# Optimization experiments

Hardware: AMD Instinct MI355X
Metric: run time of the kernel (lower is better)

Reference implementation:

```python
import jax, jax.numpy as jnp
import numpy as np

B, N, E = 2, 2048, 2048
H, D = 16, 128
BASE = 10000.0


def rope(t, offset=0):
    # t: [b, n, h, d] -- rotary position embedding (Lrpe type 1), half-rotation form
    d = t.shape[-1]
    pos = jnp.arange(t.shape[1], dtype=jnp.float32) + offset
    inv = BASE ** (-jnp.arange(0, d, 2, dtype=jnp.float32) / d)  # [d/2]
    ang = pos[:, None] * inv[None, :]                            # [n, d/2]
    cos = jnp.cos(ang)[None, :, None, :]
    sin = jnp.sin(ang)[None, :, None, :]
    t1, t2 = t[..., : d // 2], t[..., d // 2 :]
    return jnp.concatenate([t1 * cos - t2 * sin, t2 * cos + t1 * sin], axis=-1)


def setup_inputs() -> dict:
    key = jax.random.key(0)
    ks = jax.random.split(key, 6)
    s = lambda k, shape, fan: jax.random.normal(k, shape, jnp.float32) / np.sqrt(fan)
    return {
        "x": jax.random.normal(ks[0], (B, N, E), jnp.float32),
        "Wq": s(ks[1], (H * D, E), E),      # q_proj.weight
        "Wkv": s(ks[2], (2 * D, E), E),     # kv_proj.weight
        "Wkvh": s(ks[3], (2 * H, E), E),    # kv_head_proj.weight
        "Wg": s(ks[4], (2 * H, E), E),      # gate_proj.weight (gate_type=1)
        "Wout": s(ks[5], (E, H * D), H * D) # out_proj.weight
    }


def reference(x, Wq, Wkv, Wkvh, Wg, Wout):
    b, n, _ = x.shape
    q = (x @ Wq.T).reshape(b, n, H, D)
    kv = x @ Wkv.T            # [b, n, 2D]
    kv_head = x @ Wkvh.T      # [b, n, 2H] (mpa_type=0, activation 'none')

    # gate_type == 1: log-sigmoid gated cumulative-sum decay on kv_head (GLA-style)
    g = x @ Wg.T                                                       # [b, n, 2H]
    log_f = jnp.concatenate(
        [jnp.zeros((b, 1, 2 * H), jnp.float32), jax.nn.log_sigmoid(g)], axis=1
    )
    log_f_cumsum = jnp.cumsum(log_f, axis=1)[:, :-1]                   # [b, n, 2H]
    kv_head = kv_head * jnp.exp(log_f_cumsum)
    kv_head = jnp.cumsum(kv_head, axis=1)

    kp, vp = kv[..., :D], kv[..., D:]
    kh, vh = kv_head[..., :H], kv_head[..., H:]
    # low-rank KV expansion: outer product of shared (d) with per-head scalar (h)
    k = jnp.einsum('bnd,bnh->bnhd', kp, kh)
    v = jnp.einsum('bnd,bnh->bnhd', vp, vh)

    q = rope(q)
    k = rope(k)

    # causal softmax attention (flash_attn_func equivalent), scale = D**-0.5
    scale = 1.0 / np.sqrt(D)
    scores = jnp.einsum('bnhd,bmhd->bhnm', q, k) * scale
    mask = jnp.tril(jnp.ones((n, n), bool))
    scores = jnp.where(mask[None, None], scores, -jnp.inf)
    p = jax.nn.softmax(scores, axis=-1)
    o = jnp.einsum('bhnm,bmhd->bnhd', p, v).reshape(b, n, H * D)
    return o @ Wout.T
```

## Files before the change

### kernel.cpp

```cpp
#include <hip/hip_runtime.h>
#include <hip/hip_bf16.h>
#include <math.h>

typedef __attribute__((ext_vector_type(8))) short bf16x8;
typedef __attribute__((ext_vector_type(4))) float f32x4;

#define MFMA16(a, b, c) __builtin_amdgcn_mfma_f32_16x16x32_bf16((a), (b), (c), 0, 0, 0)

static __device__ __forceinline__ float fast_exp2(float x) { return __builtin_amdgcn_exp2f(x); }

static __device__ __forceinline__ unsigned short f2bf(float f) {
  __hip_bfloat16 h = __float2bfloat16(f);
  unsigned short u;
  __builtin_memcpy(&u, &h, 2);
  return u;
}
static __device__ __forceinline__ float bf2f(unsigned short u) {
  unsigned int x = ((unsigned int)u) << 16;
  float f;
  __builtin_memcpy(&f, &x, 4);
  return f;
}

static __device__ __forceinline__ void cast8(const float* __restrict__ src,
                                             unsigned short* __restrict__ dst, int blk, int tid) {
  int i = (blk * 256 + tid) * 8;
  float4 a = *(const float4*)(src + i);
  float4 b = *(const float4*)(src + i + 4);
  union { unsigned short u[8]; bf16x8 v; } o;
  o.u[0] = f2bf(a.x); o.u[1] = f2bf(a.y); o.u[2] = f2bf(a.z); o.u[3] = f2bf(a.w);
  o.u[4] = f2bf(b.x); o.u[5] = f2bf(b.y); o.u[6] = f2bf(b.z); o.u[7] = f2bf(b.w);
  *(bf16x8*)(dst + i) = o.v;
}

__global__ __launch_bounds__(256) void prep(const float* __restrict__ x, const float* __restrict__ Wq,
                                            const float* __restrict__ Wout, const float* __restrict__ Wkv,
                                            const float* __restrict__ Wkvh, const float* __restrict__ Wg,
                                            unsigned short* __restrict__ x_bf, unsigned short* __restrict__ wq_bf,
                                            unsigned short* __restrict__ wout_bf, unsigned short* __restrict__ wsm_bf,
                                            float2* __restrict__ cs, float* __restrict__ wgt) {
  int bid = blockIdx.x, tid = threadIdx.x;
  if (bid < 4096) {
    cast8(x, x_bf, bid, tid);
  } else if (bid < 6144) {
    cast8(Wq, wq_bf, bid - 4096, tid);
  } else if (bid < 8192) {
    cast8(Wout, wout_bf, bid - 6144, tid);
  } else if (bid < 8576) {
    int row = bid - 8192;
    int c = tid * 8;
    const float* src = nullptr;
    if (row < 256) src = Wkv + (size_t)row * 2048;
    else if (row < 288) src = Wkvh + (size_t)(row - 256) * 2048;
    union { unsigned short u[8]; bf16x8 v; } o;
    if (src) {
      float4 a = *(const float4*)(src + c);
      float4 b = *(const float4*)(src + c + 4);
      o.u[0] = f2bf(a.x); o.u[1] = f2bf(a.y); o.u[2] = f2bf(a.z); o.u[3] = f2bf(a.w);
      o.u[4] = f2bf(b.x); o.u[5] = f2bf(b.y); o.u[6] = f2bf(b.z); o.u[7] = f2bf(b.w);
    } else {
      for (int j = 0; j < 8; j++) o.u[j] = 0;
    }
    *(bf16x8*)(wsm_bf + (size_t)row * 2048 + c) = o.v;
  } else if (bid < 9088) {
    int i = (bid - 8576) * 256 + tid;
    int f = i & 63, n = i >> 6;
    float inv = powf(10000.0f, -(float)(2 * f) / 128.0f);
    float ang = (float)n * inv;
    cs[i] = make_float2(cosf(ang), sinf(ang));
  } else {
    int i = (bid - 9088) * 256 + tid;
    int oc = i >> 11, k = i & 2047;
    wgt[(size_t)k * 32 + oc] = Wg[i];
  }
}

__global__ __launch_bounds__(256) void gproj(const float* __restrict__ x, const float* __restrict__ Wgt,
                                             float* __restrict__ lsg_t) {
  int tid = blockIdx.x * 256 + threadIdx.x;
  int tok = tid >> 5, oc = tid & 31;
  const float* xr = x + (size_t)tok * 2048;
  float acc = 0.f;
  for (int k = 0; k < 2048; k += 4) {
    float4 a = *(const float4*)(xr + k);
    acc += a.x * Wgt[(size_t)k * 32 + oc] + a.y * Wgt[(size_t)(k + 1) * 32 + oc] +
           a.z * Wgt[(size_t)(k + 2) * 32 + oc] + a.w * Wgt[(size_t)(k + 3) * 32 + oc];
  }
  float ls = (acc >= 0.f) ? -log1pf(expf(-acc)) : acc - log1pf(expf(acc));
  int b = tok >> 11, n = tok & 2047;
  lsg_t[((size_t)(b * 32 + oc)) * 2048 + n] = ls;
}

__global__ __launch_bounds__(256) void scan_kernel(const float* __restrict__ lsg_t,
                                                   const float* __restrict__ so,
                                                   float* __restrict__ khvh) {
  int b = blockIdx.x >> 5, ch = blockIdx.x & 31;
  int t = threadIdx.x, lane = t & 63, wv = t >> 6;
  const float* L = lsg_t + ((size_t)(b * 32 + ch)) * 2048 + t * 8;
  float ls[8], v[8];
  float4 a = *(const float4*)L, c = *(const float4*)(L + 4);
  ls[0] = a.x; ls[1] = a.y; ls[2] = a.z; ls[3] = a.w;
  ls[4] = c.x; ls[5] = c.y; ls[6] = c.z; ls[7] = c.w;
  const float* V = so + ((size_t)(b * 2048 + t * 8)) * 384 + 256 + ch;
#pragma unroll
  for (int j = 0; j < 8; j++) v[j] = V[(size_t)j * 384];
  float run = 0.f;
#pragma unroll
  for (int j = 0; j < 8; j++) run += ls[j];
  float incl = run;
#pragma unroll
  for (int off = 1; off < 64; off <<= 1) {
    float nv = __shfl_up(incl, off);
    if (lane >= off) incl += nv;
  }
  __shared__ float ws[2][4];
  if (lane == 63) ws[0][wv] = incl;
  __syncthreads();
  float wbase = 0.f;
#pragma unroll
  for (int w = 0; w < 4; w++) wbase += (w < wv) ? ws[0][w] : 0.f;
  float baseA = wbase + incl - run;
  float lf = baseA, s = 0.f;
#pragma unroll
  for (int j = 0; j < 8; j++) { s += v[j] * __expf(lf); lf += ls[j]; }
  float incl2 = s;
#pragma unroll
  for (int off = 1; off < 64; off <<= 1) {
    float nv = __shfl_up(incl2, off);
    if (lane >= off) incl2 += nv;
  }
  if (lane == 63) ws[1][wv] = incl2;
  __syncthreads();
  float wbase2 = 0.f;
#pragma unroll
  for (int w = 0; w < 4; w++) wbase2 += (w < wv) ? ws[1][w] : 0.f;
  float base2 = wbase2 + incl2 - s;
  lf = baseA; s = base2;
  float* O = khvh + ((size_t)(b * 2048 + t * 8)) * 32 + ch;
#pragma unroll
  for (int j = 0; j < 8; j++) { s += v[j] * __expf(lf); lf += ls[j]; O[(size_t)j * 32] = s; }
}

__global__ __launch_bounds__(256) void build_kv2(const float* __restrict__ so,
                                                 const float* __restrict__ khvh,
                                                 const float2* __restrict__ cs,
                                                 unsigned short* __restrict__ k_r,
                                                 unsigned short* __restrict__ v_t) {
  int ntb = blockIdx.x, bh = blockIdx.y;
  int b = bh >> 4, h = bh & 15;
  int tok0 = b * 2048 + ntb * 64;
  int n0 = ntb * 64;
  __shared__ float khs[64], vhs[64];
  __shared__ unsigned short Vt_s[64 * 132];
  int t = threadIdx.x;
  if (t < 64) {
    khs[t] = khvh[(size_t)(tok0 + t) * 32 + h];
    vhs[t] = khvh[(size_t)(tok0 + t) * 32 + 16 + h];
  }
  __syncthreads();
#pragma unroll
  for (int c = 0; c < 4; c++) {
    int idx = c * 256 + t;
    int r = idx >> 4, q4 = (idx & 15) * 4;
    const float* sop = so + (size_t)(tok0 + r) * 384;
    float4 k1 = *(const float4*)(sop + q4);
    float4 k2 = *(const float4*)(sop + 64 + q4);
    float kh = khs[r];
    int n = n0 + r;
    union { unsigned short u[4]; uint2 v2; } o1, o2;
#pragma unroll
    for (int j = 0; j < 4; j++) {
      float2 cc = cs[(n << 6) + q4 + j];
      float av = ((const float*)&k1)[j], bv = ((const float*)&k2)[j];
      o1.u[j] = f2bf((av * cc.x - bv * cc.y) * kh);
      o2.u[j] = f2bf((bv * cc.x + av * cc.y) * kh);
    }
    size_t off = ((size_t)bh * 2048 + n) * 128 + q4;
    *(uint2*)(k_r + off) = o1.v2;
    *(uint2*)(k_r + off + 64) = o2.v2;
  }
#pragma unroll
  for (int c = 0; c < 8; c++) {
    int idx = c * 256 + t;
    int r = idx >> 5, d4 = (idx & 31) * 4;
    const float* sop = so + (size_t)(tok0 + r) * 384 + 128;
    float4 v = *(const float4*)(sop + d4);
    float vh = vhs[r];
    union { unsigned short u[4]; uint2 v2; } ov;
#pragma unroll
    for (int j = 0; j < 4; j++) ov.u[j] = f2bf(((const float*)&v)[j] * vh);
    *(uint2*)&Vt_s[r * 132 + d4] = ov.v2;
  }
  __syncthreads();
#pragma unroll
  for (int c = 0; c < 4; c++) {
    int idx = c * 256 + t;
    int d = idx >> 3, c8 = (idx & 7) * 8;
    union { unsigned short u[8]; bf16x8 v; } o;
#pragma unroll
    for (int j = 0; j < 8; j++) o.u[j] = Vt_s[(c8 + j) * 132 + d];
    *(bf16x8*)(v_t + ((size_t)bh * 128 + d) * 2048 + n0 + c8) = o.v;
  }
}

template <int MODE>
__global__ __launch_bounds__(256) void gemm_bt(const unsigned short* __restrict__ A,
                                               const unsigned short* __restrict__ B,
                                               float* __restrict__ Cf,
                                               unsigned short* __restrict__ Cb,
                                               int K, int ldc) {
  __shared__ unsigned short As[128 * 32];
  __shared__ unsigned short Bs[128 * 32];
  int tid = threadIdx.x;
  int wave = tid >> 6, lane = tid & 63, l15 = lane & 15, lg = lane >> 4;
  int wr = wave >> 1, wc = wave & 1;
  int lin = blockIdx.y * gridDim.x + blockIdx.x;
  int cpx = (gridDim.x * gridDim.y) >> 3;
  int swz = (lin & 7) * cpx + (lin >> 3);
  int bx = swz % gridDim.x, by = swz / gridDim.x;
  int row0 = by * 128, col0 = bx * 128;
  f32x4 acc[4][4];
#pragma unroll
  for (int m = 0; m < 4; m++)
#pragma unroll
    for (int n = 0; n < 4; n++) acc[m][n] = (f32x4){0.f, 0.f, 0.f, 0.f};

  for (int k0 = 0; k0 < K; k0 += 32) {
#pragma unroll
    for (int c = 0; c < 2; c++) {
      int chunk = c * 256 + tid;
      int r = chunk >> 2, kk = (chunk & 3) * 8;
      __builtin_amdgcn_global_load_lds(
          (const __attribute__((address_space(1))) void*)(A + (size_t)(row0 + r) * K + k0 + kk),
          (__attribute__((address_space(3))) void*)(As + ((size_t)c * 256 + wave * 64) * 8), 16, 0, 0);
      __builtin_amdgcn_global_load_lds(
          (const __attribute__((address_space(1))) void*)(B + (size_t)(col0 + r) * K + k0 + kk),
          (__attribute__((address_space(3))) void*)(Bs + ((size_t)c * 256 + wave * 64) * 8), 16, 0, 0);
    }
    __syncthreads();
    bf16x8 af[4], bfr[4];
#pragma unroll
    for (int m = 0; m < 4; m++) af[m] = *(const bf16x8*)&As[(wr * 64 + m * 16 + l15) * 32 + lg * 8];
#pragma unroll
    for (int n = 0; n < 4; n++) bfr[n] = *(const bf16x8*)&Bs[(wc * 64 + n * 16 + l15) * 32 + lg * 8];
#pragma unroll
    for (int m = 0; m < 4; m++)
#pragma unroll
      for (int n = 0; n < 4; n++) acc[m][n] = MFMA16(af[m], bfr[n], acc[m][n]);
    __syncthreads();
  }

  if (MODE == 0 || col0 >= 2048) {
#pragma unroll
    for (int m = 0; m < 4; m++) {
      int row_b = row0 + wr * 64 + m * 16 + lg * 4;
#pragma unroll
      for (int n = 0; n < 4; n++) {
        int col = col0 + wc * 64 + n * 16 + l15;
        int cw = (MODE == 0) ? col : (col - 2048);
#pragma unroll
        for (int j = 0; j < 4; j++) {
          Cf[(size_t)(row_b + j) * ldc + cw] = acc[m][n][j];
        }
      }
    }
  } else {
#pragma unroll
    for (int m = 0; m < 4; m++) {
      int row_b = row0 + wr * 64 + m * 16 + lg * 4;
#pragma unroll
      for (int n = 0; n < 4; n++) {
        int col = col0 + wc * 64 + n * 16 + l15;
        int h = col >> 7, d = col & 127;
#pragma unroll
        for (int j = 0; j < 4; j++) {
          int row = row_b + j;
          int b = row >> 11, nn = row & 2047;
          Cb[(((size_t)b * 16 + h) * 2048 + nn) * 128 + d] = f2bf(acc[m][n][j]);
        }
      }
    }
  }
}

__global__ __launch_bounds__(256, 2) void flash_attn(const unsigned short* __restrict__ q_r,
                                                     const unsigned short* __restrict__ k_r,
                                                     const unsigned short* __restrict__ v_t,
                                                     const float2* __restrict__ cs,
                                                     unsigned short* __restrict__ o) {
  int lin = blockIdx.y * 16 + blockIdx.x;
  int swz = (lin & 7) * 64 + (lin >> 3);
  int bx = swz & 15, bh = swz >> 4;
  const unsigned short* Kg = k_r + (size_t)bh * 2048 * 128;
  const unsigned short* Vtg = v_t + (size_t)bh * 128 * 2048;
  __shared__ unsigned short Ks[2][64 * 128];
  __shared__ unsigned short VTs[2][128 * 64];
  __shared__ unsigned short Ps[4][16 * 80];
  int tid = threadIdx.x, wave = tid >> 6, lane = tid & 63, l15 = lane & 15, lg = lane >> 4;
  int sw = (l15 & 7) * 8;
  int b = bh >> 4, h = bh & 15;

  union { unsigned short u[8]; bf16x8 v; } onesu;
#pragma unroll
  for (int j = 0; j < 8; j++) onesu.u[j] = 0x3F80;
  const bf16x8 ones = onesu.v;

  int qtA = bx, qtB = 31 - bx;
  int qt = qtA;

  bf16x8 qf[4];
#define LOAD_Q()                                                                                   \
  {                                                                                                \
    const unsigned short* Qg = q_r + ((size_t)bh * 2048 + qt * 64) * 128;                          \
    int n = qt * 64 + wave * 16 + l15;                                                             \
    union { unsigned short u[8]; bf16x8 v; } r0, r1, r2, r3;                                       \
    r0.v = *(const bf16x8*)(Qg + (wave * 16 + l15) * 128 + 0 * 32 + lg * 8);                       \
    r1.v = *(const bf16x8*)(Qg + (wave * 16 + l15) * 128 + 1 * 32 + lg * 8);                       \
    r2.v = *(const bf16x8*)(Qg + (wave * 16 + l15) * 128 + 2 * 32 + lg * 8);                       \
    r3.v = *(const bf16x8*)(Qg + (wave * 16 + l15) * 128 + 3 * 32 + lg * 8);                       \
    union { unsigned short u[8]; bf16x8 v; } o0, o1, o2, o3;                                       \
    _Pragma("unroll") for (int j = 0; j < 8; j++) {                                                \
      float2 c0 = cs[(n << 6) + 0 * 32 + lg * 8 + j];                                              \
      float t1 = bf2f(r0.u[j]), t2 = bf2f(r2.u[j]);                                                \
      o0.u[j] = f2bf(t1 * c0.x - t2 * c0.y);                                                       \
      o2.u[j] = f2bf(t2 * c0.x + t1 * c0.y);                                                       \
      float2 c1 = cs[(n << 6) + 1 * 32 + lg * 8 + j];                                              \
      float s1 = bf2f(r1.u[j]), s2 = bf2f(r3.u[j]);                                                \
      o1.u[j] = f2bf(s1 * c1.x - s2 * c1.y);                                                       \
      o3.u[j] = f2bf(s2 * c1.x + s1 * c1.y);                                                       \
    }                                                                                              \
    qf[0] = o0.v; qf[1] = o1.v; qf[2] = o2.v; qf[3] = o3.v;                                        \
  }

  LOAD_Q();

  float m_r[4], l_r[4];
  f32x4 oacc[8];
#pragma unroll
  for (int j = 0; j < 4; j++) { m_r[j] = -INFINITY; l_r[j] = 0.f; }
#pragma unroll
  for (int db = 0; db < 8; db++) oacc[db] = (f32x4){0.f, 0.f, 0.f, 0.f};

  const float kscale = 0.12753102f;
  const float THR = 11.0f;

#define STAGE(kt, bsel)                                                                           \
  {                                                                                               \
    int kti = (kt);                                                                               \
    int bs = (bsel);                                                                              \
    _Pragma("unroll") for (int c = 0; c < 4; c++) {                                               \
      int s = c * 256 + tid;                                                                      \
      int kr = s >> 4, kc = ((s & 15) ^ (kr & 7)) * 8;                                            \
      __builtin_amdgcn_global_load_lds(                                                           \
          (const __attribute__((address_space(1))) void*)(Kg + (size_t)(kti * 64 + kr) * 128 + kc),\
          (__attribute__((address_space(3))) void*)(&Ks[bs][(c * 256 + wave * 64) * 8]), 16, 0, 0);\
      int vr = s >> 3, vc = ((s & 7) ^ (vr & 7)) * 8;                                             \
      __builtin_amdgcn_global_load_lds(                                                           \
          (const __attribute__((address_space(1))) void*)(Vtg + (size_t)vr * 2048 + kti * 64 + vc),\
          (__attribute__((address_space(3))) void*)(&VTs[bs][(c * 256 + wave * 64) * 8]), 16, 0, 0);\
    }                                                                                             \
  }

  STAGE(0, 0);
  __syncthreads();

  for (int s = 0; s < 33; ++s) {
    int nb = s & 1;
    if (s + 1 < 33) {
      int nk = (s + 1 <= qtA) ? (s + 1) : (s + 1 - (qtA + 1));
      STAGE(nk, nb ^ 1);
    }
    int kt = (s <= qtA) ? s : (s - (qtA + 1));
    bool diag = (s == qtA) || (s == 32);
    int qrow0 = qt * 64 + wave * 16 + lg * 4;

    f32x4 sc[4];
#pragma unroll
    for (int cb = 0; cb < 4; cb++) sc[cb] = (f32x4){0.f, 0.f, 0.f, 0.f};
    __builtin_amdgcn_s_setprio(1);
#pragma unroll
    for (int kk = 0; kk < 4; kk++) {
#pragma unroll
      for (int cb = 0; cb < 4; cb++) {
        bf16x8 kf = *(const bf16x8*)&Ks[nb][(cb * 16 + l15) * 128 + ((kk * 32 + lg * 8) ^ sw)];
        sc[cb] = MFMA16(qf[kk], kf, sc[cb]);
      }
    }
    __builtin_amdgcn_s_setprio(0);
    if (diag) {
#pragma unroll
      for (int cb = 0; cb < 4; cb++) {
        int col = kt * 64 + cb * 16 + l15;
#pragma unroll
        for (int j = 0; j < 4; j++) {
          float v = sc[cb][j] * kscale;
          if (col > qrow0 + j) v = -INFINITY;
          sc[cb][j] = v;
        }
      }
    } else {
#pragma unroll
      for (int cb = 0; cb < 4; cb++)
#pragma unroll
        for (int j = 0; j < 4; j++) sc[cb][j] *= kscale;
    }
    float pm[4];
#pragma unroll
    for (int j = 0; j < 4; j++)
      pm[j] = fmaxf(fmaxf(sc[0][j], sc[1][j]), fmaxf(sc[2][j], sc[3][j]));
    bool grow = !__all((pm[0] <= m_r[0] + THR) & (pm[1] <= m_r[1] + THR) &
                       (pm[2] <= m_r[2] + THR) & (pm[3] <= m_r[3] + THR));
    if (grow) {
#pragma unroll
      for (int off = 1; off < 16; off <<= 1) {
#pragma unroll
        for (int j = 0; j < 4; j++) pm[j] = fmaxf(pm[j], __shfl_xor(pm[j], off));
      }
#pragma unroll
      for (int j = 0; j < 4; j++) {
        float mn = fmaxf(m_r[j], pm[j]);
        float corr = fast_exp2(m_r[j] - mn);
        m_r[j] = mn;
        l_r[j] *= corr;
#pragma unroll
        for (int db = 0; db < 8; db++) oacc[db][j] *= corr;
      }
    }
#pragma unroll
    for (int cb = 0; cb < 4; cb++)
#pragma unroll
      for (int j = 0; j < 4; j++)
        Ps[wave][(lg * 4 + j) * 80 + cb * 16 + l15] = f2bf(fast_exp2(sc[cb][j] - m_r[j]));
    f32x4 sacc = (f32x4){0.f, 0.f, 0.f, 0.f};
    __builtin_amdgcn_s_setprio(1);
#pragma unroll
    for (int kc = 0; kc < 2; kc++) {
      bf16x8 pa = *(const bf16x8*)&Ps[wave][l15 * 80 + kc * 32 + lg * 8];
      sacc = MFMA16(pa, ones, sacc);
#pragma unroll
      for (int db = 0; db < 8; db++) {
        bf16x8 vb = *(const bf16x8*)&VTs[nb][(db * 16 + l15) * 64 + ((kc * 32 + lg * 8) ^ sw)];
        oacc[db] = MFMA16(pa, vb, oacc[db]);
      }
    }
    __builtin_amdgcn_s_setprio(0);
#pragma unroll
    for (int j = 0; j < 4; j++) l_r[j] += sacc[j];
    __syncthreads();

    if (s == qtA) {
      int qrow_e = qt * 64 + wave * 16 + lg * 4;
#pragma unroll
      for (int db = 0; db < 8; db++) {
        int d = db * 16 + l15;
#pragma unroll
        for (int j = 0; j < 4; j++) {
          float val = oacc[db][j] / l_r[j];
          o[((size_t)(b * 2048 + qrow_e + j)) * 2048 + h * 128 + d] = f2bf(val);
        }
      }
      qt = qtB;
      LOAD_Q();
#pragma unroll
      for (int j = 0; j < 4; j++) { m_r[j] = -INFINITY; l_r[j] = 0.f; }
#pragma unroll
      for (int db = 0; db < 8; db++) oacc[db] = (f32x4){0.f, 0.f, 0.f, 0.f};
    }
  }
  int qrow_e = qt * 64 + wave * 16 + lg * 4;
#pragma unroll
  for (int db = 0; db < 8; db++) {
    int d = db * 16 + l15;
#pragma unroll
    for (int j = 0; j < 4; j++) {
      float val = oacc[db][j] / l_r[j];
      o[((size_t)(b * 2048 + qrow_e + j)) * 2048 + h * 128 + d] = f2bf(val);
    }
  }
#undef STAGE
#undef LOAD_Q
}

extern "C" void kernel_launch(void* const* d_in, const int* in_sizes, int n_in,
                              void* d_out, int out_size, void* d_ws, size_t ws_size,
                              hipStream_t stream) {
  (void)in_sizes; (void)n_in; (void)out_size; (void)ws_size;
  const float* x    = (const float*)d_in[0];
  const float* Wq   = (const float*)d_in[1];
  const float* Wkv  = (const float*)d_in[2];
  const float* Wkvh = (const float*)d_in[3];
  const float* Wg   = (const float*)d_in[4];
  const float* Wout = (const float*)d_in[5];
  float* out = (float*)d_out;

  char* ws = (char*)d_ws;
  size_t off = 0;
  auto alloc = [&](size_t bytes) -> void* {
    void* p = ws + off;
    off += (bytes + 255) & ~(size_t)255;
    return p;
  };
  unsigned short* x_bf    = (unsigned short*)alloc(4096ull * 2048 * 2);
  unsigned short* wq_bf   = (unsigned short*)alloc(2048ull * 2048 * 2);
  unsigned short* wsm_bf  = (unsigned short*)alloc(384ull * 2048 * 2);
  unsigned short* wout_bf = (unsigned short*)alloc(2048ull * 2048 * 2);
  unsigned short* q_r     = (unsigned short*)alloc(4096ull * 2048 * 2);
  unsigned short* k_r     = (unsigned short*)alloc(4096ull * 2048 * 2);
  unsigned short* o_bf    = (unsigned short*)alloc(4096ull * 2048 * 2);
  float* small_out        = (float*)alloc(4096ull * 384 * 4);
  float* lsg_t            = (float*)alloc(64ull * 2048 * 4);
  float* khvh             = (float*)alloc(4096ull * 32 * 4);
  float2* cs              = (float2*)alloc(2048ull * 64 * 8);
  float* wgt              = (float*)alloc(2048ull * 32 * 4);
  unsigned short* v_t     = x_bf;

  prep<<<9344, 256, 0, stream>>>(x, Wq, Wout, Wkv, Wkvh, Wg, x_bf, wq_bf, wout_bf, wsm_bf, cs, wgt);
  gproj<<<512, 256, 0, stream>>>(x, wgt, lsg_t);
  gemm_bt<1><<<dim3(19, 32), 256, 0, stream>>>(x_bf, wq_bf, small_out, q_r, 2048, 384);
  scan_kernel<<<64, 256, 0, stream>>>(lsg_t, small_out, khvh);
  build_kv2<<<dim3(32, 32), 256, 0, stream>>>(small_out, khvh, cs, k_r, v_t);
  flash_attn<<<dim3(16, 32), 256, 0, stream>>>(q_r, k_r, v_t, cs, o_bf);
  gemm_bt<0><<<dim3(16, 32), 256, 0, stream>>>(o_bf, wout_bf, out, nullptr, 2048, 2048);
}
```

Before: 284.0 us.

## Merge gate projection into Q GEMM launch and deepen GEMM K tile

```diff
diff --git a/kernel.cpp b/kernel.cpp
--- a/kernel.cpp
+++ b/kernel.cpp
@@ -75,20 +75,121 @@
   }
 }
 
-__global__ __launch_bounds__(256) void gproj(const float* __restrict__ x, const float* __restrict__ Wgt,
-                                             float* __restrict__ lsg_t) {
-  int tid = blockIdx.x * 256 + threadIdx.x;
-  int tok = tid >> 5, oc = tid & 31;
-  const float* xr = x + (size_t)tok * 2048;
-  float acc = 0.f;
-  for (int k = 0; k < 2048; k += 4) {
-    float4 a = *(const float4*)(xr + k);
-    acc += a.x * Wgt[(size_t)k * 32 + oc] + a.y * Wgt[(size_t)(k + 1) * 32 + oc] +
-           a.z * Wgt[(size_t)(k + 2) * 32 + oc] + a.w * Wgt[(size_t)(k + 3) * 32 + oc];
-  }
-  float ls = (acc >= 0.f) ? -log1pf(expf(-acc)) : acc - log1pf(expf(acc));
-  int b = tok >> 11, n = tok & 2047;
-  lsg_t[((size_t)(b * 32 + oc)) * 2048 + n] = ls;
+template <int MODE>
+static __device__ __forceinline__ void gemm_body(const unsigned short* __restrict__ A,
+                                                 const unsigned short* __restrict__ B,
+                                                 float* __restrict__ Cf,
+                                                 unsigned short* __restrict__ Cb,
+                                                 int K, int ldc, int lin, int nbx, int cpx) {
+  __shared__ unsigned short As[128 * 64];
+  __shared__ unsigned short Bs[128 * 64];
+  int tid = threadIdx.x;
+  int wave = tid >> 6, lane = tid & 63, l15 = lane & 15, lg = lane >> 4;
+  int wr = wave >> 1, wc = wave & 1;
+  int swz = (lin & 7) * cpx + (lin >> 3);
+  int bx = swz % nbx, by = swz / nbx;
+  int row0 = by * 128, col0 = bx * 128;
+  f32x4 acc[4][4];
+#pragma unroll
+  for (int m = 0; m < 4; m++)
+#pragma unroll
+    for (int n = 0; n < 4; n++) acc[m][n] = (f32x4){0.f, 0.f, 0.f, 0.f};
+
+  for (int k0 = 0; k0 < K; k0 += 64) {
+#pragma unroll
+    for (int c = 0; c < 4; c++) {
+      int chunk = c * 256 + tid;
+      int r = chunk >> 3, kk = (chunk & 7) * 8;
+      __builtin_amdgcn_global_load_lds(
+          (const __attribute__((address_space(1))) void*)(A + (size_t)(row0 + r) * K + k0 + kk),
+          (__attribute__((address_space(3))) void*)(As + ((size_t)c * 256 + wave * 64) * 8), 16, 0, 0);
+      __builtin_amdgcn_global_load_lds(
+          (const __attribute__((address_space(1))) void*)(B + (size_t)(col0 + r) * K + k0 + kk),
+          (__attribute__((address_space(3))) void*)(Bs + ((size_t)c * 256 + wave * 64) * 8), 16, 0, 0);
+    }
+    __syncthreads();
+    bf16x8 af[4][2], bfr[4][2];
+#pragma unroll
+    for (int m = 0; m < 4; m++)
+#pragma unroll
+      for (int ks = 0; ks < 2; ks++)
+        af[m][ks] = *(const bf16x8*)&As[(wr * 64 + m * 16 + l15) * 64 + ks * 32 + lg * 8];
+#pragma unroll
+    for (int n = 0; n < 4; n++)
+#pragma unroll
+      for (int ks = 0; ks < 2; ks++)
+        bfr[n][ks] = *(const bf16x8*)&Bs[(wc * 64 + n * 16 + l15) * 64 + ks * 32 + lg * 8];
+#pragma unroll
+    for (int ks = 0; ks < 2; ks++)
+#pragma unroll
+      for (int m = 0; m < 4; m++)
+#pragma unroll
+        for (int n = 0; n < 4; n++) acc[m][n] = MFMA16(af[m][ks], bfr[n][ks], acc[m][n]);
+    __syncthreads();
+  }
+
+  if (MODE == 0 || col0 >= 2048) {
+#pragma unroll
+    for (int m = 0; m < 4; m++) {
+      int row_b = row0 + wr * 64 + m * 16 + lg * 4;
+#pragma unroll
+      for (int n = 0; n < 4; n++) {
+        int col = col0 + wc * 64 + n * 16 + l15;
+        int cw = (MODE == 0) ? col : (col - 2048);
+#pragma unroll
+        for (int j = 0; j < 4; j++) {
+          Cf[(size_t)(row_b + j) * ldc + cw] = acc[m][n][j];
+        }
+      }
+    }
+  } else {
+#pragma unroll
+    for (int m = 0; m < 4; m++) {
+      int row_b = row0 + wr * 64 + m * 16 + lg * 4;
+#pragma unroll
+      for (int n = 0; n < 4; n++) {
+        int col = col0 + wc * 64 + n * 16 + l15;
+        int h = col >> 7, d = col & 127;
+#pragma unroll
+        for (int j = 0; j < 4; j++) {
+          int row = row_b + j;
+          int b = row >> 11, nn = row & 2047;
+          Cb[(((size_t)b * 16 + h) * 2048 + nn) * 128 + d] = f2bf(acc[m][n][j]);
+        }
+      }
+    }
+  }
+}
+
+__global__ __launch_bounds__(256) void gemm_q_gproj(const unsigned short* __restrict__ A,
+                                                    const unsigned short* __restrict__ B,
+                                                    float* __restrict__ small_out,
+                                                    unsigned short* __restrict__ q_r,
+                                                    const float* __restrict__ x,
+                                                    const float* __restrict__ Wgt,
+                                                    float* __restrict__ lsg_t) {
+  if (blockIdx.x >= 608) {
+    int tid = (blockIdx.x - 608) * 256 + threadIdx.x;
+    int tok = tid >> 5, oc = tid & 31;
+    const float* xr = x + (size_t)tok * 2048;
+    float acc = 0.f;
+    for (int k = 0; k < 2048; k += 4) {
+      float4 a = *(const float4*)(xr + k);
+      acc += a.x * Wgt[(size_t)k * 32 + oc] + a.y * Wgt[(size_t)(k + 1) * 32 + oc] +
+             a.z * Wgt[(size_t)(k + 2) * 32 + oc] + a.w * Wgt[(size_t)(k + 3) * 32 + oc];
+    }
+    float ls = (acc >= 0.f) ? -log1pf(expf(-acc)) : acc - log1pf(expf(acc));
+    int b = tok >> 11, n = tok & 2047;
+    lsg_t[((size_t)(b * 32 + oc)) * 2048 + n] = ls;
+    return;
+  }
+  gemm_body<1>(A, B, small_out, q_r, 2048, 384, blockIdx.x, 19, 76);
+}
+
+__global__ __launch_bounds__(256) void gemm_out(const unsigned short* __restrict__ A,
+                                                const unsigned short* __restrict__ B,
+                                                float* __restrict__ C) {
+  gemm_body<0>(A, B, C, nullptr, 2048, 2048, (int)(blockIdx.y * 16 + blockIdx.x), 16, 64);
 }
 
 __global__ __launch_bounds__(256) void scan_kernel(const float* __restrict__ lsg_t,
@@ -203,86 +304,6 @@
   }
 }
 
-template <int MODE>
-__global__ __launch_bounds__(256) void gemm_bt(const unsigned short* __restrict__ A,
-                                               const unsigned short* __restrict__ B,
-                                               float* __restrict__ Cf,
-                                               unsigned short* __restrict__ Cb,
-                                               int K, int ldc) {
-  __shared__ unsigned short As[128 * 32];
-  __shared__ unsigned short Bs[128 * 32];
-  int tid = threadIdx.x;
-  int wave = tid >> 6, lane = tid & 63, l15 = lane & 15, lg = lane >> 4;
-  int wr = wave >> 1, wc = wave & 1;
-  int lin = blockIdx.y * gridDim.x + blockIdx.x;
-  int cpx = (gridDim.x * gridDim.y) >> 3;
-  int swz = (lin & 7) * cpx + (lin >> 3);
-  int bx = swz % gridDim.x, by = swz / gridDim.x;
-  int row0 = by * 128, col0 = bx * 128;
-  f32x4 acc[4][4];
-#pragma unroll
-  for (int m = 0; m < 4; m++)
-#pragma unroll
-    for (int n = 0; n < 4; n++) acc[m][n] = (f32x4){0.f, 0.f, 0.f, 0.f};
-
-  for (int k0 = 0; k0 < K; k0 += 32) {
-#pragma unroll
-    for (int c = 0; c < 2; c++) {
-      int chunk = c * 256 + tid;
-      int r = chunk >> 2, kk = (chunk & 3) * 8;
-      __builtin_amdgcn_global_load_lds(
-          (const __attribute__((address_space(1))) void*)(A + (size_t)(row0 + r) * K + k0 + kk),
-          (__attribute__((address_space(3))) void*)(As + ((size_t)c * 256 + wave * 64) * 8), 16, 0, 0);
-      __builtin_amdgcn_global_load_lds(
-          (const __attribute__((address_space(1))) void*)(B + (size_t)(col0 + r) * K + k0 + kk),
-          (__attribute__((address_space(3))) void*)(Bs + ((size_t)c * 256 + wave * 64) * 8), 16, 0, 0);
-    }
-    __syncthreads();
-    bf16x8 af[4], bfr[4];
-#pragma unroll
-    for (int m = 0; m < 4; m++) af[m] = *(const bf16x8*)&As[(wr * 64 + m * 16 + l15) * 32 + lg * 8];
-#pragma unroll
-    for (int n = 0; n < 4; n++) bfr[n] = *(const bf16x8*)&Bs[(wc * 64 + n * 16 + l15) * 32 + lg * 8];
-#pragma unroll
-    for (int m = 0; m < 4; m++)
-#pragma unroll
-      for (int n = 0; n < 4; n++) acc[m][n] = MFMA16(af[m], bfr[n], acc[m][n]);
-    __syncthreads();
-  }
-
-  if (MODE == 0 || col0 >= 2048) {
-#pragma unroll
-    for (int m = 0; m < 4; m++) {
-      int row_b = row0 + wr * 64 + m * 16 + lg * 4;
-#pragma unroll
-      for (int n = 0; n < 4; n++) {
-        int col = col0 + wc * 64 + n * 16 + l15;
-        int cw = (MODE == 0) ? col : (col - 2048);
-#pragma unroll
-        for (int j = 0; j < 4; j++) {
-          Cf[(size_t)(row_b + j) * ldc + cw] = acc[m][n][j];
-        }
-      }
-    }
-  } else {
-#pragma unroll
-    for (int m = 0; m < 4; m++) {
-      int row_b = row0 + wr * 64 + m * 16 + lg * 4;
-#pragma unroll
-      for (int n = 0; n < 4; n++) {
-        int col = col0 + wc * 64 + n * 16 + l15;
-        int h = col >> 7, d = col & 127;
-#pragma unroll
-        for (int j = 0; j < 4; j++) {
-          int row = row_b + j;
-          int b = row >> 11, nn = row & 2047;
-          Cb[(((size_t)b * 16 + h) * 2048 + nn) * 128 + d] = f2bf(acc[m][n][j]);
-        }
-      }
-    }
-  }
-}
-
 __global__ __launch_bounds__(256, 2) void flash_attn(const unsigned short* __restrict__ q_r,
                                                      const unsigned short* __restrict__ k_r,
                                                      const unsigned short* __restrict__ v_t,
@@ -295,7 +316,7 @@
   const unsigned short* Vtg = v_t + (size_t)bh * 128 * 2048;
   __shared__ unsigned short Ks[2][64 * 128];
   __shared__ unsigned short VTs[2][128 * 64];
-  __shared__ unsigned short Ps[4][16 * 80];
+  __shared__ unsigned short Ps[4][16 * 72];
   int tid = threadIdx.x, wave = tid >> 6, lane = tid & 63, l15 = lane & 15, lg = lane >> 4;
   int sw = (l15 & 7) * 8;
   int b = bh >> 4, h = bh & 15;
@@ -430,12 +451,12 @@
     for (int cb = 0; cb < 4; cb++)
 #pragma unroll
       for (int j = 0; j < 4; j++)
-        Ps[wave][(lg * 4 + j) * 80 + cb * 16 + l15] = f2bf(fast_exp2(sc[cb][j] - m_r[j]));
+        Ps[wave][(lg * 4 + j) * 72 + cb * 16 + l15] = f2bf(fast_exp2(sc[cb][j] - m_r[j]));
     f32x4 sacc = (f32x4){0.f, 0.f, 0.f, 0.f};
     __builtin_amdgcn_s_setprio(1);
 #pragma unroll
     for (int kc = 0; kc < 2; kc++) {
-      bf16x8 pa = *(const bf16x8*)&Ps[wave][l15 * 80 + kc * 32 + lg * 8];
+      bf16x8 pa = *(const bf16x8*)&Ps[wave][l15 * 72 + kc * 32 + lg * 8];
       sacc = MFMA16(pa, ones, sacc);
 #pragma unroll
       for (int db = 0; db < 8; db++) {
@@ -515,10 +536,9 @@
   unsigned short* v_t     = x_bf;
 
   prep<<<9344, 256, 0, stream>>>(x, Wq, Wout, Wkv, Wkvh, Wg, x_bf, wq_bf, wout_bf, wsm_bf, cs, wgt);
-  gproj<<<512, 256, 0, stream>>>(x, wgt, lsg_t);
-  gemm_bt<1><<<dim3(19, 32), 256, 0, stream>>>(x_bf, wq_bf, small_out, q_r, 2048, 384);
+  gemm_q_gproj<<<1120, 256, 0, stream>>>(x_bf, wq_bf, small_out, q_r, x, wgt, lsg_t);
   scan_kernel<<<64, 256, 0, stream>>>(lsg_t, small_out, khvh);
   build_kv2<<<dim3(32, 32), 256, 0, stream>>>(small_out, khvh, cs, k_r, v_t);
   flash_attn<<<dim3(16, 32), 256, 0, stream>>>(q_r, k_r, v_t, cs, o_bf);
-  gemm_bt<0><<<dim3(16, 32), 256, 0, stream>>>(o_bf, wout_bf, out, nullptr, 2048, 2048);
-}
+  gemm_out<<<dim3(16, 32), 256, 0, stream>>>(o_bf, wout_bf, out);
+}
```

Measured after the change: 297.1 us. 4.6% more time.
